# Optimization experiments

Measured on AMD Instinct MI355X. Metric: run time of the kernel, lower is better.

## Reference

```python
import jax, jax.numpy as jnp
import numpy as np

WS = 8  # window_size
EPS = 1e-5  # BatchNorm eps


def setup_inputs() -> dict:
    key = jax.random.key(0)
    ks = jax.random.split(key, 11)
    c = 64
    return {
        "x": jax.random.normal(ks[0], (4, c, 256, 256), dtype=jnp.float32),
        "w_in": jax.random.normal(ks[1], (c, c), dtype=jnp.float32) * 0.05,
        "b_in": jax.random.normal(ks[2], (c,), dtype=jnp.float32) * 0.05,
        "bn_gamma": jax.random.uniform(ks[3], (c,), dtype=jnp.float32),
        "bn_beta": jax.random.normal(ks[4], (c,), dtype=jnp.float32) * 0.05,
        "bn_mean": jax.random.normal(ks[5], (c,), dtype=jnp.float32) * 0.05,
        "bn_var": jax.random.uniform(ks[6], (c,), dtype=jnp.float32),
        "w_mask": jax.random.normal(ks[7], (c, c), dtype=jnp.float32) * 0.05,
        "b_mask": jax.random.normal(ks[8], (c,), dtype=jnp.float32) * 0.05,
        "w_out": jax.random.normal(ks[9], (c, c), dtype=jnp.float32) * 0.05,
        "b_out": jax.random.normal(ks[10], (c,), dtype=jnp.float32) * 0.05,
    }


def reference(x, w_in, b_in, bn_gamma, bn_beta, bn_mean, bn_var,
              w_mask, b_mask, w_out, b_out):
    ws = WS
    b, c, h, w = x.shape  # shifts == 0 -> no roll

    # project_inp: 1x1 conv + BatchNorm2d (inference mode, running stats)
    x = jnp.einsum('bchw,oc->bohw', x, w_in) + b_in[None, :, None, None]
    inv = bn_gamma / jnp.sqrt(bn_var + EPS)
    x = (x - bn_mean[None, :, None, None]) * inv[None, :, None, None] \
        + bn_beta[None, :, None, None]

    # seq_refl_win_pad(back=False): pad right/bottom by ws, then copy the
    # preceding ws rows into the bottom pad, then the preceding ws cols
    # (including the new bottom rows) into the right pad.
    x_pad = jnp.concatenate([x, x[:, :, -ws:, :]], axis=2)      # [b,c,h+ws,w]
    x_pad = jnp.concatenate([x_pad, x_pad[:, :, :, -ws:]], axis=3)  # [b,c,h+ws,w+ws]

    hh, ww = h // ws, w // ws
    # mask = Conv2d(kernel=1, stride=2) on the 2ws x 2ws windows ->
    # equivalent to sampling even offsets inside each window, then a 1x1 linear.
    row = (jnp.arange(hh) * ws)[:, None] + jnp.arange(0, 2 * ws, 2)[None, :]  # [hh, ws]
    col = (jnp.arange(ww) * ws)[:, None] + jnp.arange(0, 2 * ws, 2)[None, :]  # [ww, ws]
    g = x_pad[:, :, row, :]        # [b, c, hh, ws_h, w+ws]
    g = g[:, :, :, :, col]         # [b, c, hh, ws_h, ww, ws_w]
    # torch's double unfold yields window dims ordered (W-window, H-window),
    # and q flattens in that (Wwin, Hwin) order -> match exactly.
    g = jnp.transpose(g, (0, 2, 4, 5, 3, 1))        # [b, hh, ww, ws_w, ws_h, c]
    q = g.reshape(b * hh * ww, ws * ws, c)
    q = q @ w_mask.T + b_mask                       # 1x1 conv as per-pixel linear

    # v: non-overlapping ws x ws windows of x, flattened H-major (dh dw)
    v = x.reshape(b, c, hh, ws, ww, ws)
    v = jnp.transpose(v, (0, 2, 4, 3, 5, 1)).reshape(b * hh * ww, ws * ws, c)

    atn = jax.nn.softmax(q @ jnp.swapaxes(q, -1, -2), axis=-1)  # [bn, ws^2, ws^2]
    y = atn @ v                                                  # [bn, ws^2, c]

    # reassemble: '(b h w) (dh dw) c -> b c (h dh) (w dw)'
    y = y.reshape(b, hh, ww, ws, ws, c)
    y = jnp.transpose(y, (0, 5, 1, 3, 2, 4)).reshape(b, c, h, w)

    # project_out: 1x1 conv
    y = jnp.einsum('bchw,oc->bohw', y, w_out) + b_out[None, :, None, None]
    return y
```

## Files before the change

### kernel.cpp

```cpp
#include <hip/hip_runtime.h>

typedef unsigned short ushort_t;
typedef unsigned int uint_t;
typedef __attribute__((ext_vector_type(8))) short short8v;
typedef __attribute__((ext_vector_type(4))) float f32x4;

__device__ __forceinline__ float bf2f(ushort_t u) {
    union { uint_t u; float f; } v; v.u = (uint_t)u << 16; return v.f;
}
__device__ __forceinline__ ushort_t f2bf(float f) {
    union { float f; uint_t u; } v; v.f = f;
    uint_t u = v.u;
    return (ushort_t)((u + 0x7fffu + ((u >> 16) & 1u)) >> 16);
}

#define MFMA(A,B,C) __builtin_amdgcn_mfma_f32_16x16x32_bf16(A, B, C, 0, 0, 0)

__device__ __forceinline__ void split8(float4 f0, float4 f1, short8v& h8, short8v& l8) {
    float v[8] = {f0.x, f0.y, f0.z, f0.w, f1.x, f1.y, f1.z, f1.w};
    union { short8v v; ushort_t s[8]; } H, L;
    #pragma unroll
    for (int e = 0; e < 8; ++e) {
        ushort_t h = f2bf(v[e]);
        H.s[e] = h;
        L.s[e] = f2bf(v[e] - bf2f(h));
    }
    h8 = H.v; l8 = L.v;
}

__global__ __launch_bounds__(256, 4) void k1_pwbn_mfma(
    const float* __restrict__ x, const float* __restrict__ w_in, const float* __restrict__ b_in,
    const float* __restrict__ gamma, const float* __restrict__ beta,
    const float* __restrict__ mean, const float* __restrict__ var,
    ushort_t* __restrict__ xbn)
{
    __shared__ short xsh[64][72];
    __shared__ short xsl[64][72];
    __shared__ short wfh[64][72];
    __shared__ short wfl[64][72];
    __shared__ float bef[64];

    int tid = threadIdx.x;
    int b   = blockIdx.x >> 10;
    int hw0 = (blockIdx.x & 1023) << 6;
    const float* xb = x + ((size_t)b << 22);

    #pragma unroll
    for (int u = 0; u < 2; ++u) {
        int idx = u * 256 + tid;
        int cp = idx >> 4, pq = idx & 15;
        int c0 = cp * 2, p0 = pq * 4;
        float4 fa = *(const float4*)(xb + (size_t)c0 * 65536 + hw0 + p0);
        float4 fb = *(const float4*)(xb + (size_t)(c0 + 1) * 65536 + hw0 + p0);
        float va[4] = {fa.x, fa.y, fa.z, fa.w};
        float vb[4] = {fb.x, fb.y, fb.z, fb.w};
        #pragma unroll
        for (int e = 0; e < 4; ++e) {
            ushort_t h0 = f2bf(va[e]), h1 = f2bf(vb[e]);
            ushort_t l0 = f2bf(va[e] - bf2f(h0)), l1 = f2bf(vb[e] - bf2f(h1));
            *(uint_t*)&xsh[p0 + e][c0] = (uint_t)h0 | ((uint_t)h1 << 16);
            *(uint_t*)&xsl[p0 + e][c0] = (uint_t)l0 | ((uint_t)l1 << 16);
        }
    }
    #pragma unroll
    for (int v = 0; v < 2; ++v) {
        int idx = v * 256 + tid;
        int o = idx >> 3, c0 = (idx & 7) * 8;
        float sc = gamma[o] * rsqrtf(var[o] + 1e-5f);
        float4 fa = *(const float4*)(w_in + o * 64 + c0);
        float4 fb = *(const float4*)(w_in + o * 64 + c0 + 4);
        float vv[8] = {fa.x, fa.y, fa.z, fa.w, fb.x, fb.y, fb.z, fb.w};
        union { int4 q; ushort_t s[8]; } ph, pl;
        #pragma unroll
        for (int e = 0; e < 8; ++e) {
            float wv = vv[e] * sc;
            ushort_t h = f2bf(wv);
            ph.s[e] = h;
            pl.s[e] = f2bf(wv - bf2f(h));
        }
        *(int4*)&wfh[o][c0] = ph.q;
        *(int4*)&wfl[o][c0] = pl.q;
    }
    if (tid < 64) {
        float inv = gamma[tid] * rsqrtf(var[tid] + 1e-5f);
        bef[tid] = (b_in[tid] - mean[tid]) * inv + beta[tid];
    }
    __syncthreads();

    int w = tid >> 6, l = tid & 63;
    int half = l >> 4, lr = l & 15;
    int k0 = half * 8;

    short8v bh[2], bl[2];
    #pragma unroll
    for (int kc = 0; kc < 2; ++kc) {
        bh[kc] = *(short8v*)&xsh[16 * w + lr][k0 + 32 * kc];
        bl[kc] = *(short8v*)&xsl[16 * w + lr][k0 + 32 * kc];
    }
    short8v ah[4][2], al[4][2];
    #pragma unroll
    for (int ot = 0; ot < 4; ++ot)
        #pragma unroll
        for (int kc = 0; kc < 2; ++kc) {
            ah[ot][kc] = *(short8v*)&wfh[16 * ot + lr][k0 + 32 * kc];
            al[ot][kc] = *(short8v*)&wfl[16 * ot + lr][k0 + 32 * kc];
        }

    ushort_t* xp = xbn + ((size_t)(b * 65536 + hw0 + 16 * w + lr) << 6);
    #pragma unroll
    for (int ot = 0; ot < 4; ++ot) {
        f32x4 acc = {0.f, 0.f, 0.f, 0.f};
        #pragma unroll
        for (int kc = 0; kc < 2; ++kc) {
            acc = MFMA(ah[ot][kc], bh[kc], acc);
            acc = MFMA(ah[ot][kc], bl[kc], acc);
            acc = MFMA(al[ot][kc], bh[kc], acc);
        }
        int o0 = 16 * ot + 4 * half;
        float4 bq = *(const float4*)&bef[o0];
        float bqs[4] = {bq.x, bq.y, bq.z, bq.w};
        ushort_t hs[4];
        #pragma unroll
        for (int rr = 0; rr < 4; ++rr) hs[rr] = f2bf(acc[rr] + bqs[rr]);
        *(uint2*)(xp + o0) = make_uint2((uint_t)hs[0] | ((uint_t)hs[1] << 16),
                                        (uint_t)hs[2] | ((uint_t)hs[3] << 16));
    }
}

#define K4_G    0
#define K4_V    9216
#define K4_QH   18432
#define K4_QL   27648
#define K4_RED  36864
#define K4_RED2 37888
#define K4_TOT  38912

__global__ __launch_bounds__(256, 4) void k2_attn_v4(
    const ushort_t* __restrict__ xbn,
    const float* __restrict__ w_mask, const float* __restrict__ b_mask,
    const float* __restrict__ w_out,  const float* __restrict__ b_out,
    float* __restrict__ out)
{
    __shared__ char smem[K4_TOT];
    short* gb   = (short*)(smem + K4_G);
    short* vb   = (short*)(smem + K4_V);
    short* qhb  = (short*)(smem + K4_QH);
    short* qlb  = (short*)(smem + K4_QL);
    short* vwt  = (short*)(smem + K4_G);
    short* pt   = (short*)(smem + K4_V);
    float* outt = (float*)(smem + K4_QH);
    float* red  = (float*)(smem + K4_RED);
    float* red2 = (float*)(smem + K4_RED2);

    int tid = threadIdx.x;
    int wid = blockIdx.x;
    int b = wid >> 10, i = (wid >> 5) & 31, j = wid & 31;
    const ushort_t* xb = xbn + ((size_t)b << 22);

    int w = tid >> 6, l = tid & 63;
    int half = l >> 4, lr = l & 15;
    int mrow = (16 * w + lr) * 72;
    int kc0 = half * 8, kc1 = 32 + half * 8;

    const float* wmp = w_mask + (16 * w + lr) * 64;
    const float* wop = w_out  + (16 * w + lr) * 64;
    float4 wmA = *(const float4*)(wmp + kc0), wmB = *(const float4*)(wmp + kc0 + 4);
    float4 wmC = *(const float4*)(wmp + kc1), wmD = *(const float4*)(wmp + kc1 + 4);
    float4 woA = *(const float4*)(wop + kc0), woB = *(const float4*)(wop + kc0 + 4);
    float4 woC = *(const float4*)(wop + kc1), woD = *(const float4*)(wop + kc1 + 4);

    {
        int t = tid >> 2, seg = tid & 3;
        int r = t & 7, s = t >> 3;
        int pr = i * 8 + 2 * r; if (pr >= 256) pr -= 8;
        int pc = j * 8 + 2 * s; if (pc >= 256) pc -= 8;
        const ushort_t* src = xb + (((size_t)((pr << 8) | pc)) << 6) + seg * 16;
        *(int4*)(gb + t * 72 + seg * 16)     = *(const int4*)src;
        *(int4*)(gb + t * 72 + seg * 16 + 8) = *(const int4*)(src + 8);
        int vr = i * 8 + (t >> 3), vc = j * 8 + (t & 7);
        const ushort_t* vsrc = xb + (((size_t)((vr << 8) | vc)) << 6) + seg * 16;
        *(int4*)(vb + t * 72 + seg * 16)     = *(const int4*)vsrc;
        *(int4*)(vb + t * 72 + seg * 16 + 8) = *(const int4*)(vsrc + 8);
    }
    __syncthreads();

    {
        short8v amh0, aml0, amh1, aml1;
        split8(wmA, wmB, amh0, aml0);
        split8(wmC, wmD, amh1, aml1);
        float4 bm = *(const float4*)(b_mask + 16 * w + half * 4);
        float bmv[4] = {bm.x, bm.y, bm.z, bm.w};
        #pragma unroll
        for (int n = 0; n < 4; ++n) {
            int nrow = (16 * n + lr) * 72;
            short8v bg0 = *(short8v*)(gb + nrow + kc0);
            short8v bg1 = *(short8v*)(gb + nrow + kc1);
            f32x4 acc = {0.f, 0.f, 0.f, 0.f};
            acc = MFMA(amh0, bg0, acc);
            acc = MFMA(amh1, bg1, acc);
            acc = MFMA(aml0, bg0, acc);
            acc = MFMA(aml1, bg1, acc);
            ushort_t hs[4], ls[4];
            #pragma unroll
            for (int rr = 0; rr < 4; ++rr) {
                float qv = acc[rr] + bmv[rr];
                hs[rr] = f2bf(qv);
                ls[rr] = f2bf(qv - bf2f(hs[rr]));
            }
            int qoff = (16 * n + lr) * 72 + 16 * w + half * 4;
            *(uint2*)(qhb + qoff) = make_uint2((uint_t)hs[0] | ((uint_t)hs[1] << 16),
                                               (uint_t)hs[2] | ((uint_t)hs[3] << 16));
            *(uint2*)(qlb + qoff) = make_uint2((uint_t)ls[0] | ((uint_t)ls[1] << 16),
                                               (uint_t)ls[2] | ((uint_t)ls[3] << 16));
        }
    }
    __syncthreads();

    {
        short8v bh0, bl0, bh1, bl1;
        split8(woA, woB, bh0, bl0);
        split8(woC, woD, bh1, bl1);
        #pragma unroll
        for (int mm = 0; mm < 4; ++mm) {
            int arow = (16 * mm + lr) * 72;
            short8v av0 = *(short8v*)(vb + arow + kc0);
            short8v av1 = *(short8v*)(vb + arow + kc1);
            f32x4 acc = {0.f, 0.f, 0.f, 0.f};
            acc = MFMA(av0, bh0, acc);
            acc = MFMA(av1, bh1, acc);
            acc = MFMA(av0, bl0, acc);
            acc = MFMA(av1, bl1, acc);
            ushort_t hs[4];
            #pragma unroll
            for (int rr = 0; rr < 4; ++rr) hs[rr] = f2bf(acc[rr]);
            int voff = (16 * w + lr) * 72 + 16 * mm + 4 * half;
            *(uint2*)(vwt + voff) = make_uint2((uint_t)hs[0] | ((uint_t)hs[1] << 16),
                                               (uint_t)hs[2] | ((uint_t)hs[3] << 16));
        }
    }
    f32x4 sreg[4];
    {
        short8v ah0 = *(short8v*)(qhb + mrow + kc0);
        short8v ah1 = *(short8v*)(qhb + mrow + kc1);
        short8v al0 = *(short8v*)(qlb + mrow + kc0);
        short8v al1 = *(short8v*)(qlb + mrow + kc1);
        #pragma unroll
        for (int n = 0; n < 4; ++n) {
            int nrow = (16 * n + lr) * 72;
            short8v bh0 = *(short8v*)(qhb + nrow + kc0);
            short8v bh1 = *(short8v*)(qhb + nrow + kc1);
            short8v bl0 = *(short8v*)(qlb + nrow + kc0);
            short8v bl1 = *(short8v*)(qlb + nrow + kc1);
            f32x4 acc = {0.f, 0.f, 0.f, 0.f};
            acc = MFMA(ah0, bh0, acc);
            acc = MFMA(ah1, bh1, acc);
            acc = MFMA(ah0, bl0, acc);
            acc = MFMA(ah1, bl1, acc);
            acc = MFMA(al0, bh0, acc);
            acc = MFMA(al1, bh1, acc);
            sreg[n] = acc;
        }
        #pragma unroll
        for (int n = 0; n < 4; ++n) {
            float pm = fmaxf(fmaxf(sreg[n][0], sreg[n][1]), fmaxf(sreg[n][2], sreg[n][3]));
            pm = fmaxf(pm, __shfl_xor(pm, 16));
            pm = fmaxf(pm, __shfl_xor(pm, 32));
            if (half == 0) red[(16 * n + lr) * 4 + w] = pm;
        }
    }
    __syncthreads();

    {
        #pragma unroll
        for (int n = 0; n < 4; ++n) {
            int t = 16 * n + lr;
            float4 r4 = *(const float4*)&red[t * 4];
            float m = fmaxf(fmaxf(r4.x, r4.y), fmaxf(r4.z, r4.w));
            ushort_t hs[4];
            float ps = 0.f;
            #pragma unroll
            for (int rr = 0; rr < 4; ++rr) {
                ushort_t h = f2bf(__expf(sreg[n][rr] - m));
                ps += bf2f(h);
                hs[rr] = h;
            }
            *(uint2*)(pt + t * 72 + 16 * w + 4 * half) =
                make_uint2((uint_t)hs[0] | ((uint_t)hs[1] << 16),
                           (uint_t)hs[2] | ((uint_t)hs[3] << 16));
            ps += __shfl_xor(ps, 16);
            ps += __shfl_xor(ps, 32);
            if (half == 0) red2[t * 4 + w] = ps;
        }
    }
    __syncthreads();

    {
        short8v bv0 = *(short8v*)(vwt + mrow + kc0);
        short8v bv1 = *(short8v*)(vwt + mrow + kc1);
        float bo = b_out[16 * w + lr];
        int swz = lr & 7;
        #pragma unroll
        for (int mm = 0; mm < 4; ++mm) {
            int arow = (16 * mm + lr) * 72;
            short8v ap0 = *(short8v*)(pt + arow + kc0);
            short8v ap1 = *(short8v*)(pt + arow + kc1);
            f32x4 acc = {0.f, 0.f, 0.f, 0.f};
            acc = MFMA(ap0, bv0, acc);
            acc = MFMA(ap1, bv1, acc);
            f32x4 wv;
            #pragma unroll
            for (int rr = 0; rr < 4; ++rr) {
                int t = 16 * mm + 4 * half + rr;
                float4 s4 = *(const float4*)&red2[t * 4];
                float inv = 1.0f / (s4.x + s4.y + s4.z + s4.w);
                wv[rr] = acc[rr] * inv + bo;
            }
            int c4s = (4 * mm + half) ^ swz;
            *(f32x4*)(outt + (16 * w + lr) * 64 + c4s * 4) = wv;
        }
    }
    __syncthreads();

    {
        float* ob = out + ((size_t)b << 22);
        int base = (i * 8) * 256 + j * 8;
        for (int pp = 0; pp < 16; ++pp) {
            int e = pp * 256 + tid;
            int o = e >> 6, t = e & 63;
            float val = outt[o * 64 + (((t >> 2) ^ (o & 7)) << 2) + (t & 3)];
            ob[((size_t)o << 16) + base + ((t >> 3) << 8) + (t & 7)] = val;
        }
    }
}

extern "C" void kernel_launch(void* const* d_in, const int* in_sizes, int n_in,
                              void* d_out, int out_size, void* d_ws, size_t ws_size,
                              hipStream_t stream) {
    const float* x      = (const float*)d_in[0];
    const float* w_in   = (const float*)d_in[1];
    const float* b_in   = (const float*)d_in[2];
    const float* gamma  = (const float*)d_in[3];
    const float* beta   = (const float*)d_in[4];
    const float* mean   = (const float*)d_in[5];
    const float* var    = (const float*)d_in[6];
    const float* w_mask = (const float*)d_in[7];
    const float* b_mask = (const float*)d_in[8];
    const float* w_out  = (const float*)d_in[9];
    const float* b_out  = (const float*)d_in[10];
    float* out = (float*)d_out;
    ushort_t* xbn = (ushort_t*)d_ws;

    hipLaunchKernelGGL(k1_pwbn_mfma, dim3(4096), dim3(256), 0, stream,
                       x, w_in, b_in, gamma, beta, mean, var, xbn);
    hipLaunchKernelGGL(k2_attn_v4, dim3(4096), dim3(256), 0, stream,
                       xbn, w_mask, b_mask, w_out, b_out, out);
}
```

Measured before the change: 186.9 us.

## Drop LDS staging in projection kernels, load operands and store outputs directly

The first kernel no longer stages x and the folded weights through shared memory. Each lane gathers its MFMA operands straight from global memory with scalar strided loads and folds in BatchNorm per output. The second kernel swaps the operand order of the final out-projection MFMA so each lane writes its results directly to global memory, removing the LDS transpose buffer and one barrier. The bf16 rounding helper now uses the HIP intrinsic. The cost is less coalesced global access (scalar loads strided by channel in k1, 4-byte scattered stores in k2) and redundant per-lane weight conversion.

```diff
diff --git a/kernel.cpp b/kernel.cpp
--- a/kernel.cpp
+++ b/kernel.cpp
@@ -1,4 +1,5 @@
 #include <hip/hip_runtime.h>
+#include <hip/hip_bf16.h>
 
 typedef unsigned short ushort_t;
 typedef unsigned int uint_t;
@@ -9,9 +10,8 @@
     union { uint_t u; float f; } v; v.u = (uint_t)u << 16; return v.f;
 }
 __device__ __forceinline__ ushort_t f2bf(float f) {
-    union { float f; uint_t u; } v; v.f = f;
-    uint_t u = v.u;
-    return (ushort_t)((u + 0x7fffu + ((u >> 16) & 1u)) >> 16);
+    __hip_bfloat16 h = __float2bfloat16(f);
+    return *reinterpret_cast<ushort_t*>(&h);
 }
 
 #define MFMA(A,B,C) __builtin_amdgcn_mfma_f32_16x16x32_bf16(A, B, C, 0, 0, 0)
@@ -28,100 +28,83 @@
     h8 = H.v; l8 = L.v;
 }
 
-__global__ __launch_bounds__(256, 4) void k1_pwbn_mfma(
+__global__ __launch_bounds__(256, 4) void k1_pwbn_direct(
     const float* __restrict__ x, const float* __restrict__ w_in, const float* __restrict__ b_in,
     const float* __restrict__ gamma, const float* __restrict__ beta,
     const float* __restrict__ mean, const float* __restrict__ var,
     ushort_t* __restrict__ xbn)
 {
-    __shared__ short xsh[64][72];
-    __shared__ short xsl[64][72];
-    __shared__ short wfh[64][72];
-    __shared__ short wfl[64][72];
-    __shared__ float bef[64];
-
     int tid = threadIdx.x;
     int b   = blockIdx.x >> 10;
     int hw0 = (blockIdx.x & 1023) << 6;
     const float* xb = x + ((size_t)b << 22);
 
-    #pragma unroll
-    for (int u = 0; u < 2; ++u) {
-        int idx = u * 256 + tid;
-        int cp = idx >> 4, pq = idx & 15;
-        int c0 = cp * 2, p0 = pq * 4;
-        float4 fa = *(const float4*)(xb + (size_t)c0 * 65536 + hw0 + p0);
-        float4 fb = *(const float4*)(xb + (size_t)(c0 + 1) * 65536 + hw0 + p0);
-        float va[4] = {fa.x, fa.y, fa.z, fa.w};
-        float vb[4] = {fb.x, fb.y, fb.z, fb.w};
-        #pragma unroll
-        for (int e = 0; e < 4; ++e) {
-            ushort_t h0 = f2bf(va[e]), h1 = f2bf(vb[e]);
-            ushort_t l0 = f2bf(va[e] - bf2f(h0)), l1 = f2bf(vb[e] - bf2f(h1));
-            *(uint_t*)&xsh[p0 + e][c0] = (uint_t)h0 | ((uint_t)h1 << 16);
-            *(uint_t*)&xsl[p0 + e][c0] = (uint_t)l0 | ((uint_t)l1 << 16);
-        }
-    }
-    #pragma unroll
-    for (int v = 0; v < 2; ++v) {
-        int idx = v * 256 + tid;
-        int o = idx >> 3, c0 = (idx & 7) * 8;
-        float sc = gamma[o] * rsqrtf(var[o] + 1e-5f);
-        float4 fa = *(const float4*)(w_in + o * 64 + c0);
-        float4 fb = *(const float4*)(w_in + o * 64 + c0 + 4);
-        float vv[8] = {fa.x, fa.y, fa.z, fa.w, fb.x, fb.y, fb.z, fb.w};
-        union { int4 q; ushort_t s[8]; } ph, pl;
-        #pragma unroll
-        for (int e = 0; e < 8; ++e) {
-            float wv = vv[e] * sc;
-            ushort_t h = f2bf(wv);
-            ph.s[e] = h;
-            pl.s[e] = f2bf(wv - bf2f(h));
-        }
-        *(int4*)&wfh[o][c0] = ph.q;
-        *(int4*)&wfl[o][c0] = pl.q;
-    }
-    if (tid < 64) {
-        float inv = gamma[tid] * rsqrtf(var[tid] + 1e-5f);
-        bef[tid] = (b_in[tid] - mean[tid]) * inv + beta[tid];
-    }
-    __syncthreads();
-
     int w = tid >> 6, l = tid & 63;
     int half = l >> 4, lr = l & 15;
     int k0 = half * 8;
+    int px = hw0 + 16 * w + lr;
 
     short8v bh[2], bl[2];
     #pragma unroll
     for (int kc = 0; kc < 2; ++kc) {
-        bh[kc] = *(short8v*)&xsh[16 * w + lr][k0 + 32 * kc];
-        bl[kc] = *(short8v*)&xsl[16 * w + lr][k0 + 32 * kc];
-    }
-    short8v ah[4][2], al[4][2];
-    #pragma unroll
-    for (int ot = 0; ot < 4; ++ot)
-        #pragma unroll
-        for (int kc = 0; kc < 2; ++kc) {
-            ah[ot][kc] = *(short8v*)&wfh[16 * ot + lr][k0 + 32 * kc];
-            al[ot][kc] = *(short8v*)&wfl[16 * ot + lr][k0 + 32 * kc];
-        }
-
-    ushort_t* xp = xbn + ((size_t)(b * 65536 + hw0 + 16 * w + lr) << 6);
+        union { short8v v; ushort_t s[8]; } H, L;
+        #pragma unroll
+        for (int e = 0; e < 8; ++e) {
+            float xv = xb[((32 * kc + k0 + e) << 16) + px];
+            ushort_t h = f2bf(xv);
+            H.s[e] = h;
+            L.s[e] = f2bf(xv - bf2f(h));
+        }
+        bh[kc] = H.v; bl[kc] = L.v;
+    }
+
+    ushort_t* xp = xbn + ((size_t)(b * 65536 + px) << 6);
     #pragma unroll
     for (int ot = 0; ot < 4; ++ot) {
+        int o = 16 * ot + lr;
+        float sc = gamma[o] * rsqrtf(var[o] + 1e-5f);
+        short8v ah[2], al[2];
+        #pragma unroll
+        for (int kc = 0; kc < 2; ++kc) {
+            float4 fa = *(const float4*)(w_in + o * 64 + 32 * kc + k0);
+            float4 fb = *(const float4*)(w_in + o * 64 + 32 * kc + k0 + 4);
+            float vv[8] = {fa.x, fa.y, fa.z, fa.w, fb.x, fb.y, fb.z, fb.w};
+            union { short8v v; ushort_t s[8]; } H, L;
+            #pragma unroll
+            for (int e = 0; e < 8; ++e) {
+                float wv = vv[e] * sc;
+                ushort_t h = f2bf(wv);
+                H.s[e] = h;
+                L.s[e] = f2bf(wv - bf2f(h));
+            }
+            ah[kc] = H.v; al[kc] = L.v;
+        }
+
         f32x4 acc = {0.f, 0.f, 0.f, 0.f};
         #pragma unroll
         for (int kc = 0; kc < 2; ++kc) {
-            acc = MFMA(ah[ot][kc], bh[kc], acc);
-            acc = MFMA(ah[ot][kc], bl[kc], acc);
-            acc = MFMA(al[ot][kc], bh[kc], acc);
+            acc = MFMA(ah[kc], bh[kc], acc);
+            acc = MFMA(ah[kc], bl[kc], acc);
+            acc = MFMA(al[kc], bh[kc], acc);
         }
         int o0 = 16 * ot + 4 * half;
-        float4 bq = *(const float4*)&bef[o0];
-        float bqs[4] = {bq.x, bq.y, bq.z, bq.w};
+        float4 g4 = *(const float4*)(gamma + o0);
+        float4 v4 = *(const float4*)(var + o0);
+        float4 bi4 = *(const float4*)(b_in + o0);
+        float4 mn4 = *(const float4*)(mean + o0);
+        float4 bt4 = *(const float4*)(beta + o0);
+        float gv[4] = {g4.x, g4.y, g4.z, g4.w};
+        float vv2[4] = {v4.x, v4.y, v4.z, v4.w};
+        float bi[4] = {bi4.x, bi4.y, bi4.z, bi4.w};
+        float mn[4] = {mn4.x, mn4.y, mn4.z, mn4.w};
+        float bt[4] = {bt4.x, bt4.y, bt4.z, bt4.w};
         ushort_t hs[4];
         #pragma unroll
-        for (int rr = 0; rr < 4; ++rr) hs[rr] = f2bf(acc[rr] + bqs[rr]);
+        for (int rr = 0; rr < 4; ++rr) {
+            float inv = gv[rr] * rsqrtf(vv2[rr] + 1e-5f);
+            float bef = (bi[rr] - mn[rr]) * inv + bt[rr];
+            hs[rr] = f2bf(acc[rr] + bef);
+        }
         *(uint2*)(xp + o0) = make_uint2((uint_t)hs[0] | ((uint_t)hs[1] << 16),
                                         (uint_t)hs[2] | ((uint_t)hs[3] << 16));
     }
@@ -135,7 +118,7 @@
 #define K4_RED2 37888
 #define K4_TOT  38912
 
-__global__ __launch_bounds__(256, 4) void k2_attn_v4(
+__global__ __launch_bounds__(256, 4) void k2_attn_v5(
     const ushort_t* __restrict__ xbn,
     const float* __restrict__ w_mask, const float* __restrict__ b_mask,
     const float* __restrict__ w_out,  const float* __restrict__ b_out,
@@ -148,7 +131,6 @@
     short* qlb  = (short*)(smem + K4_QL);
     short* vwt  = (short*)(smem + K4_G);
     short* pt   = (short*)(smem + K4_V);
-    float* outt = (float*)(smem + K4_QH);
     float* red  = (float*)(smem + K4_RED);
     float* red2 = (float*)(smem + K4_RED2);
 
@@ -295,40 +277,29 @@
     __syncthreads();
 
     {
-        short8v bv0 = *(short8v*)(vwt + mrow + kc0);
-        short8v bv1 = *(short8v*)(vwt + mrow + kc1);
-        float bo = b_out[16 * w + lr];
-        int swz = lr & 7;
-        #pragma unroll
-        for (int mm = 0; mm < 4; ++mm) {
-            int arow = (16 * mm + lr) * 72;
-            short8v ap0 = *(short8v*)(pt + arow + kc0);
-            short8v ap1 = *(short8v*)(pt + arow + kc1);
-            f32x4 acc = {0.f, 0.f, 0.f, 0.f};
-            acc = MFMA(ap0, bv0, acc);
-            acc = MFMA(ap1, bv1, acc);
-            f32x4 wv;
-            #pragma unroll
-            for (int rr = 0; rr < 4; ++rr) {
-                int t = 16 * mm + 4 * half + rr;
-                float4 s4 = *(const float4*)&red2[t * 4];
-                float inv = 1.0f / (s4.x + s4.y + s4.z + s4.w);
-                wv[rr] = acc[rr] * inv + bo;
-            }
-            int c4s = (4 * mm + half) ^ swz;
-            *(f32x4*)(outt + (16 * w + lr) * 64 + c4s * 4) = wv;
-        }
-    }
-    __syncthreads();
-
-    {
+        short8v a0 = *(short8v*)(vwt + mrow + kc0);
+        short8v a1 = *(short8v*)(vwt + mrow + kc1);
         float* ob = out + ((size_t)b << 22);
         int base = (i * 8) * 256 + j * 8;
-        for (int pp = 0; pp < 16; ++pp) {
-            int e = pp * 256 + tid;
-            int o = e >> 6, t = e & 63;
-            float val = outt[o * 64 + (((t >> 2) ^ (o & 7)) << 2) + (t & 3)];
-            ob[((size_t)o << 16) + base + ((t >> 3) << 8) + (t & 7)] = val;
+        float4 bo4 = *(const float4*)(b_out + 16 * w + 4 * half);
+        float bov[4] = {bo4.x, bo4.y, bo4.z, bo4.w};
+        #pragma unroll
+        for (int n = 0; n < 4; ++n) {
+            int trow = (16 * n + lr) * 72;
+            short8v p0 = *(short8v*)(pt + trow + kc0);
+            short8v p1 = *(short8v*)(pt + trow + kc1);
+            f32x4 acc = {0.f, 0.f, 0.f, 0.f};
+            acc = MFMA(a0, p0, acc);
+            acc = MFMA(a1, p1, acc);
+            int t = 16 * n + lr;
+            float4 s4 = *(const float4*)&red2[t * 4];
+            float inv = 1.0f / (s4.x + s4.y + s4.z + s4.w);
+            size_t paddr = base + ((t >> 3) << 8) + (t & 7);
+            #pragma unroll
+            for (int rr = 0; rr < 4; ++rr) {
+                int o = 16 * w + 4 * half + rr;
+                ob[((size_t)o << 16) + paddr] = acc[rr] * inv + bov[rr];
+            }
         }
     }
 }
@@ -350,8 +321,8 @@
     float* out = (float*)d_out;
     ushort_t* xbn = (ushort_t*)d_ws;
 
-    hipLaunchKernelGGL(k1_pwbn_mfma, dim3(4096), dim3(256), 0, stream,
+    hipLaunchKernelGGL(k1_pwbn_direct, dim3(4096), dim3(256), 0, stream,
                        x, w_in, b_in, gamma, beta, mean, var, xbn);
-    hipLaunchKernelGGL(k2_attn_v4, dim3(4096), dim3(256), 0, stream,
+    hipLaunchKernelGGL(k2_attn_v5, dim3(4096), dim3(256), 0, stream,
                        xbn, w_mask, b_mask, w_out, b_out, out);
 }
```

Measured after the change: 208.7 us. 1.12x slower.
